# Kernel optimization log

Measured on AMD Instinct MI355X. Metric: run time of the kernel, lower is better.

The kernel has to match this reference:

```python
import jax, jax.numpy as jnp
import numpy as np

N = 8192   # max_nodes
E = 8192   # max_edges
D = 128    # node / edge feature dim


def setup_inputs() -> dict:
    key = jax.random.key(0)
    ks = jax.random.split(key, 6)
    nodes = jax.random.normal(ks[0], (N, D), jnp.float32)
    edges = jax.random.normal(ks[1], (E, D), jnp.float32)
    send = jax.random.randint(ks[2], (E,), 0, N, jnp.int32)
    rec = jax.random.randint(ks[3], (E,), 0, N, jnp.int32)
    # prefix activity masks (standard for this growing-graph module)
    anodes = (jnp.arange(N) < 6144).astype(jnp.float32)
    aedges = (jnp.arange(E) < 2048).astype(jnp.float32)
    Wq = jax.random.normal(ks[4], (D, D), jnp.float32) / np.sqrt(D)
    bq = jnp.zeros((D,), jnp.float32)
    Wp = jax.random.normal(ks[5], (D, 1), jnp.float32) * 0.1
    bp = jnp.full((1,), -5.0, jnp.float32)
    return dict(nodes=nodes, edges=edges, rec=rec, send=send, anodes=anodes,
                aedges=aedges, Wq=Wq, bq=bq, Wp=Wp, bp=bp)


def reference(nodes, edges, rec, send, anodes, aedges, Wq, bq, Wp, bp):
    # fixed PRNG key (the module takes a key argument; we pin it for determinism)
    key = jax.random.key(42)
    key_prob, key_edges, key_samp = jax.random.split(key, 3)

    nids = jnp.arange(N)
    e_active = aedges.sum().astype(jnp.int32)

    # 1. per-node edge-generation probability: prob_fn(h_i) = sigmoid(h_i @ Wp + bp)
    probs = jax.nn.sigmoid(nodes @ Wp + bp)[:, 0]            # [N]
    # 2. sample generating nodes (only active ones)
    gens = (jax.random.uniform(key_prob, (N,)) < probs * anodes).astype(jnp.float32)

    allowed = E - e_active - 1
    n_gens = jnp.clip(gens.astype(jnp.int32).sum(), 0, allowed)

    # grow active-edge mask by n_gens via repeated (mask @ incr_matrix) clip steps
    # incr_matrix(E) = I + superdiagonal, so one step extends a prefix mask by 1
    mat_e = jnp.eye(E, dtype=jnp.float32) + jnp.eye(E, k=1, dtype=jnp.float32)
    naedges = jax.lax.fori_loop(
        0, n_gens, lambda i, x: jnp.clip(x @ mat_e, 0.0, 1.0), aedges
    ).at[-1].set(0.0)
    mask_new = naedges * (1.0 - aedges)                       # [E] newly-created slots

    # 6. new edges get random embeddings in the newly-activated slots
    new_edges = edges + jax.random.normal(key_edges, edges.shape) * mask_new[:, None]

    # cumsum-derived scatter targets: k-th generating node -> edge slot e_active+k
    gi = gens.astype(jnp.int32)
    trgets = jnp.where(gens > 0, (jnp.cumsum(gens) * gens - gens).astype(jnp.int32), -1) \
             + e_active * gi                                   # [N], -1 dropped by segment_sum

    nsend = jax.ops.segment_sum(nids, trgets, num_segments=E)
    nsend = (send * (1.0 - mask_new) + nsend).astype(jnp.int32)

    # 3-5. queries, all-pairs scores, masked categorical target sampling
    queries = nodes @ Wq + bq                                  # [N, D]
    scores = jnp.clip(queries @ nodes.T, -1e4, 1e4)            # [N, N]
    scores = scores - (1.0 - anodes[None, :]) * 1e10
    select = jnp.where(gens > 0,
                       jax.random.categorical(key_samp, scores, axis=-1),
                       0).astype(jnp.int32)                    # [N]

    nrec = jax.ops.segment_sum(select, trgets, num_segments=E)
    nrec = (rec * (1.0 - mask_new) + nrec).astype(jnp.int32)

    return new_edges, nsend, nrec, naedges
```

## Files before the change

### kernel.cpp

```cpp
#include <hip/hip_runtime.h>
#include <stdint.h>
#include <math.h>

#define NN 8192
#define EE 8192
#define DD 128

__host__ __device__ inline void tf2x32(uint32_t k0, uint32_t k1, uint32_t c0, uint32_t c1,
                                       uint32_t& o0, uint32_t& o1) {
  uint32_t ks[3] = {k0, k1, 0x1BD11BDAu ^ k0 ^ k1};
  uint32_t x0 = c0 + k0, x1 = c1 + k1;
  const uint32_t rot0[4] = {13u, 15u, 26u, 6u};
  const uint32_t rot1[4] = {17u, 29u, 16u, 24u};
#pragma unroll
  for (int i = 0; i < 5; ++i) {
#pragma unroll
    for (int r = 0; r < 4; ++r) {
      uint32_t d = (i & 1) ? rot1[r] : rot0[r];
      x0 += x1;
      x1 = (x1 << d) | (x1 >> (32u - d));
      x1 ^= x0;
    }
    x0 += ks[(i + 1) % 3];
    x1 += ks[(i + 2) % 3] + (uint32_t)(i + 1);
  }
  o0 = x0; o1 = x1;
}

__device__ inline uint32_t rbits32(uint32_t k0, uint32_t k1, uint32_t idx) {
  uint32_t o0, o1;
  tf2x32(k0, k1, 0u, idx, o0, o1);
  return o0 ^ o1;
}

__device__ inline float u01(uint32_t b) {
  return __uint_as_float((b >> 9) | 0x3f800000u) - 1.0f;
}

__device__ inline float erfinv_f32(float x) {
  float w = -log1pf(-x * x);
  float p;
  if (w < 5.0f) {
    w -= 2.5f;
    p = 2.81022636e-08f;
    p = fmaf(p, w, 3.43273939e-07f);
    p = fmaf(p, w, -3.5233877e-06f);
    p = fmaf(p, w, -4.39150654e-06f);
    p = fmaf(p, w, 0.00021858087f);
    p = fmaf(p, w, -0.00125372503f);
    p = fmaf(p, w, -0.00417768164f);
    p = fmaf(p, w, 0.246640727f);
    p = fmaf(p, w, 1.50140941f);
  } else {
    w = sqrtf(w) - 3.0f;
    p = -0.000200214257f;
    p = fmaf(p, w, 0.000100950558f);
    p = fmaf(p, w, 0.00134934322f);
    p = fmaf(p, w, -0.00367342844f);
    p = fmaf(p, w, 0.00573950773f);
    p = fmaf(p, w, -0.0076224613f);
    p = fmaf(p, w, 0.00943887047f);
    p = fmaf(p, w, 1.00167406f);
    p = fmaf(p, w, 2.83297682f);
  }
  return p * x;
}

__global__ __launch_bounds__(256)
void k_gens(const float* __restrict__ nodes, const float* __restrict__ Wp,
            const float* __restrict__ bp, const float* __restrict__ anodes,
            int* __restrict__ gens, uint32_t kp0, uint32_t kp1) {
  int t = blockIdx.x * 256 + threadIdx.x;
  int i = t >> 2, qd = t & 3;
  if (i >= NN) return;
  const float4* row = (const float4*)(nodes + (size_t)i * DD);
  const float4* w = (const float4*)Wp;
  float acc = 0.f;
#pragma unroll
  for (int c = 0; c < 8; ++c) {
    int k4 = qd + 4 * c;
    float4 a = row[k4], b = w[k4];
    acc = fmaf(a.x, b.x, acc); acc = fmaf(a.y, b.y, acc);
    acc = fmaf(a.z, b.z, acc); acc = fmaf(a.w, b.w, acc);
  }
  acc += __shfl_xor(acc, 1, 4);
  acc += __shfl_xor(acc, 2, 4);
  if (qd == 0) {
    float prob = 1.0f / (1.0f + expf(-(acc + bp[0])));
    uint32_t b = rbits32(kp0, kp1, (uint32_t)i);
    gens[i] = (u01(b) < prob * anodes[i]) ? 1 : 0;
  }
}

__global__ __launch_bounds__(256)
void k_scan(const float* __restrict__ aedges, const int* __restrict__ gens,
            int* __restrict__ gen_list, float* __restrict__ mask_new,
            float* __restrict__ naedges_out, int* __restrict__ scal,
            unsigned long long* __restrict__ partial) {
  __shared__ int P[EE];
  __shared__ int aux[8];
  int tid = threadIdx.x;
  int base = tid * 32;
  int lane = tid & 63, wid = tid >> 6;

  int av[32]; int aloc = 0;
  {
    const float4* a4 = (const float4*)(aedges + base);
#pragma unroll
    for (int k4 = 0; k4 < 8; ++k4) {
      float4 x = a4[k4];
      av[4 * k4 + 0] = (x.x > 0.f); av[4 * k4 + 1] = (x.y > 0.f);
      av[4 * k4 + 2] = (x.z > 0.f); av[4 * k4 + 3] = (x.w > 0.f);
    }
#pragma unroll
    for (int k = 0; k < 32; ++k) aloc += av[k];
  }
  int incl = aloc;
#pragma unroll
  for (int d = 1; d < 64; d <<= 1) {
    int o = __shfl_up(incl, d, 64);
    if (lane >= d) incl += o;
  }
  if (lane == 63) aux[wid] = incl;

  int g[32]; int gloc = 0;
  {
    const int4* g4 = (const int4*)(gens + base);
#pragma unroll
    for (int k4 = 0; k4 < 8; ++k4) {
      int4 x = g4[k4];
      g[4 * k4 + 0] = x.x; g[4 * k4 + 1] = x.y;
      g[4 * k4 + 2] = x.z; g[4 * k4 + 3] = x.w;
    }
#pragma unroll
    for (int k = 0; k < 32; ++k) gloc += g[k];
  }
  int incg = gloc;
#pragma unroll
  for (int d = 1; d < 64; d <<= 1) {
    int o = __shfl_up(incg, d, 64);
    if (lane >= d) incg += o;
  }
  if (lane == 63) aux[4 + wid] = incg;
  __syncthreads();

  int e_active = aux[0] + aux[1] + aux[2] + aux[3];
  int total = aux[4] + aux[5] + aux[6] + aux[7];
  int wpreA = 0, wpreG = 0;
  for (int ww = 0; ww < wid; ++ww) { wpreA += aux[ww]; wpreG += aux[4 + ww]; }

  {
    int run = wpreA + incl - aloc;
#pragma unroll
    for (int k = 0; k < 32; ++k) { run += av[k]; P[base + k] = run; }
  }
  {
    int rank = wpreG + incg - gloc;
#pragma unroll
    for (int k = 0; k < 32; ++k) {
      if (g[k]) {
        if (e_active + rank < EE) gen_list[rank] = base + k;
        rank++;
      }
    }
  }
  if (tid == 0) { scal[0] = e_active; scal[1] = total; }

  for (int idx = tid; idx < total * 32; idx += 256) partial[idx] = 0ull;

  int allowed = EE - e_active - 1;
  int n_gens = total;
  if (n_gens > allowed) n_gens = allowed;
  if (n_gens < 0) n_gens = 0;

  __syncthreads();
#pragma unroll
  for (int k = 0; k < 32; ++k) {
    int j = base + k;
    int lo = j - n_gens - 1;
    int wsum = P[j] - (lo >= 0 ? P[lo] : 0);
    float dil = (wsum > 0) ? 1.f : 0.f;
    if (j == EE - 1) dil = 0.f;
    naedges_out[j] = dil;
    mask_new[j] = dil * (1.0f - (float)av[k]);
  }
}

__global__ __launch_bounds__(128)
void k_queries(const float* __restrict__ nodes, const float* __restrict__ Wq,
               const float* __restrict__ bq, const int* __restrict__ gen_list,
               const int* __restrict__ scal, float* __restrict__ queries) {
  __shared__ float ni[DD];
  int tid = threadIdx.x;
  int total = scal[1];
  for (int r = blockIdx.x; r < total; r += gridDim.x) {
    int i = gen_list[r];
    ni[tid] = nodes[(size_t)i * DD + tid];
    __syncthreads();
    float acc = bq[tid];
    for (int k = 0; k < DD; ++k) acc = fmaf(ni[k], Wq[k * DD + tid], acc);
    queries[(size_t)r * DD + tid] = acc;
    __syncthreads();
  }
}

__global__ __launch_bounds__(256)
void k_score(const float* __restrict__ nodes, const float* __restrict__ anodes,
             const float* __restrict__ queries, const int* __restrict__ gen_list,
             const int* __restrict__ scal, unsigned long long* __restrict__ partial,
             uint32_t ks0, uint32_t ks1) {
  __shared__ float4 nd[32][32];
  __shared__ float q[8][DD];
  __shared__ float an[32];
  __shared__ int gi[8];
  int tid = threadIdx.x;
  int j0 = blockIdx.x * 32;
  int total = scal[1];
  int rt0 = blockIdx.y * 8;
  if (rt0 >= total) return;

  {
    int jj = tid >> 3, sub = tid & 7;
    const float4* src = (const float4*)(nodes + (size_t)(j0 + jj) * DD);
#pragma unroll
    for (int c = 0; c < 4; ++c) {
      int k4 = sub + 8 * c;
      nd[jj][k4 ^ (jj & 7)] = src[k4];
    }
    if (tid < 32) an[tid] = anodes[j0 + tid];
  }

  int rr = tid >> 5, jj = tid & 31;
  for (int rb = rt0; rb < total; rb += 8 * gridDim.y) {
    __syncthreads();
    {
      int lr = rb + (tid >> 5);
      int k4 = tid & 31;
      if (lr < total) {
        ((float4*)q[tid >> 5])[k4] = ((const float4*)(queries + (size_t)lr * DD))[k4];
        if (k4 == 0) gi[tid >> 5] = gen_list[lr];
      }
    }
    __syncthreads();

    int r = rb + rr;
    if (r < total) {
      const float4* qv = (const float4*)q[rr];
      float acc = 0.f;
#pragma unroll
      for (int k4 = 0; k4 < 32; ++k4) {
        float4 n = nd[jj][k4 ^ (jj & 7)];
        float4 qq = qv[k4];
        acc = fmaf(n.x, qq.x, acc); acc = fmaf(n.y, qq.y, acc);
        acc = fmaf(n.z, qq.z, acc); acc = fmaf(n.w, qq.w, acc);
      }
      int j = j0 + jj;
      float sc = fminf(fmaxf(acc, -1e4f), 1e4f);
      sc -= (1.0f - an[jj]) * 1e10f;
      uint32_t bidx = (uint32_t)gi[rr] * NN + (uint32_t)j;
      uint32_t b = rbits32(ks0, ks1, bidx);
      float u = fmaxf(1.17549435e-38f, u01(b));
      float gmb = -logf(-logf(u));
      float v = sc + gmb;
      int jbest = j;
#pragma unroll
      for (int m = 16; m; m >>= 1) {
        float ov = __shfl_xor(v, m, 32);
        int oj = __shfl_xor(jbest, m, 32);
        if (ov > v || (ov == v && oj < jbest)) { v = ov; jbest = oj; }
      }
      if (jj == 0) {
        uint32_t fb = __float_as_uint(v);
        fb = (fb & 0x80000000u) ? ~fb : (fb | 0x80000000u);
        unsigned long long key =
            ((unsigned long long)fb << 32) | (uint32_t)(NN - 1 - jbest);
        atomicMax(&partial[(size_t)r * 32 + (blockIdx.x >> 3)], key);
      }
    }
  }
}

__global__ __launch_bounds__(256)
void k_post(const float* __restrict__ edges, const float* __restrict__ mask_new,
            const int* __restrict__ send, const int* __restrict__ rec,
            const int* __restrict__ gen_list,
            const unsigned long long* __restrict__ partial,
            const int* __restrict__ scal,
            float* __restrict__ out_edges, float* __restrict__ out_nsend,
            float* __restrict__ out_nrec, uint32_t ke0, uint32_t ke1) {
  int t = blockIdx.x * 256 + threadIdx.x;
  int idx = t * 4;
  int e = idx >> 7;
  float m = mask_new[e];
  float4 v = ((const float4*)edges)[t];
  if (m > 0.f) {
    float* pv = &v.x;
#pragma unroll
    for (int k = 0; k < 4; ++k) {
      uint32_t b = rbits32(ke0, ke1, (uint32_t)(idx + k));
      float u = u01(b);
      float x = fmaf(u, 2.0f, -0.99999994f);
      x = fmaxf(-0.99999994f, x);
      float nrm = 1.41421354f * erfinv_f32(x);
      pv[k] += nrm * m;
    }
  }
  ((float4*)out_edges)[t] = v;

  if (t < EE) {
    int e_active = scal[0], total = scal[1];
    float mm = mask_new[t];
    float sf = (float)send[t] * (1.0f - mm);
    float rf = (float)rec[t] * (1.0f - mm);
    int r = t - e_active;
    if (r >= 0 && r < total) {
      unsigned long long best = 0ull;
      const unsigned long long* pp = partial + (size_t)r * 32;
#pragma unroll
      for (int p = 0; p < 32; ++p) { unsigned long long x = pp[p]; if (x > best) best = x; }
      int i = gen_list[r];
      int jsel = (NN - 1) - (int)(best & 0xFFFFFFFFull);
      sf += (float)i;
      rf += (float)jsel;
    }
    out_nsend[t] = (float)(int)sf;
    out_nrec[t] = (float)(int)rf;
  }
}

extern "C" void kernel_launch(void* const* d_in, const int* in_sizes, int n_in,
                              void* d_out, int out_size, void* d_ws, size_t ws_size,
                              hipStream_t stream) {
  const float* nodes  = (const float*)d_in[0];
  const float* edges  = (const float*)d_in[1];
  const int*   rec    = (const int*)d_in[2];
  const int*   send   = (const int*)d_in[3];
  const float* anodes = (const float*)d_in[4];
  const float* aedges = (const float*)d_in[5];
  const float* Wq     = (const float*)d_in[6];
  const float* bq     = (const float*)d_in[7];
  const float* Wp     = (const float*)d_in[8];
  const float* bp     = (const float*)d_in[9];

  float* out        = (float*)d_out;
  float* out_edges  = out;
  float* out_nsend  = out + (size_t)EE * DD;
  float* out_nrec   = out_nsend + EE;
  float* out_naedge = out_nrec + EE;

  char* w = (char*)d_ws;
  int*   gens     = (int*)w;
  int*   gen_list = (int*)(w + 32768);
  int*   scal     = (int*)(w + 65536);
  float* mask_new = (float*)(w + 65792);
  unsigned long long* partial = (unsigned long long*)(w + 98560);
  float* queries  = (float*)(w + 98560 + 6144 * 32 * 8);

  uint32_t kp0, kp1, ke0, ke1, ks0, ks1;
  tf2x32(0u, 42u, 0u, 0u, kp0, kp1);
  tf2x32(0u, 42u, 0u, 1u, ke0, ke1);
  tf2x32(0u, 42u, 0u, 2u, ks0, ks1);

  k_gens<<<NN * 4 / 256, 256, 0, stream>>>(nodes, Wp, bp, anodes, gens, kp0, kp1);
  k_scan<<<1, 256, 0, stream>>>(aedges, gens, gen_list, mask_new, out_naedge, scal, partial);
  k_queries<<<128, 128, 0, stream>>>(nodes, Wq, bq, gen_list, scal, queries);
  k_score<<<dim3(NN / 32, 16), 256, 0, stream>>>(nodes, anodes, queries, gen_list, scal,
                                                 partial, ks0, ks1);
  k_post<<<(EE * DD / 4) / 256, 256, 0, stream>>>(edges, mask_new, send, rec, gen_list,
                                                  partial, scal, out_edges, out_nsend,
                                                  out_nrec, ke0, ke1);
}
```

Baseline: 44.81 us.

## Fuse score and post kernels with grid-wide completion counter

Result: slower. 68.71 us (+53.4%).

```diff
diff --git a/kernel.cpp b/kernel.cpp
--- a/kernel.cpp
+++ b/kernel.cpp
@@ -5,6 +5,7 @@
 #define NN 8192
 #define EE 8192
 #define DD 128
+#define FGRID 1280
 
 __host__ __device__ inline void tf2x32(uint32_t k0, uint32_t k1, uint32_t c0, uint32_t c1,
                                        uint32_t& o0, uint32_t& o1) {
@@ -96,7 +97,7 @@
 void k_scan(const float* __restrict__ aedges, const int* __restrict__ gens,
             int* __restrict__ gen_list, float* __restrict__ mask_new,
             float* __restrict__ naedges_out, int* __restrict__ scal,
-            unsigned long long* __restrict__ partial) {
+            unsigned long long* __restrict__ partial, int* __restrict__ done) {
   __shared__ int P[EE];
   __shared__ int aux[8];
   int tid = threadIdx.x;
@@ -164,7 +165,7 @@
       }
     }
   }
-  if (tid == 0) { scal[0] = e_active; scal[1] = total; }
+  if (tid == 0) { scal[0] = e_active; scal[1] = total; *done = 0; }
 
   for (int idx = tid; idx < total * 32; idx += 256) partial[idx] = 0ull;
 
@@ -204,111 +205,122 @@
   }
 }
 
-__global__ __launch_bounds__(256)
-void k_score(const float* __restrict__ nodes, const float* __restrict__ anodes,
+__global__ __launch_bounds__(256, 5)
+void k_fused(const float* __restrict__ nodes, const float* __restrict__ anodes,
              const float* __restrict__ queries, const int* __restrict__ gen_list,
              const int* __restrict__ scal, unsigned long long* __restrict__ partial,
-             uint32_t ks0, uint32_t ks1) {
-  __shared__ float4 nd[32][32];
+             int* __restrict__ done,
+             const float* __restrict__ edges, const float* __restrict__ mask_new,
+             const int* __restrict__ send, const int* __restrict__ rec,
+             float* __restrict__ out_edges, float* __restrict__ out_nsend,
+             float* __restrict__ out_nrec,
+             uint32_t ks0, uint32_t ks1, uint32_t ke0, uint32_t ke1) {
+  __shared__ float4 nd[32 * 32];
   __shared__ float q[8][DD];
   __shared__ float an[32];
   __shared__ int gi[8];
   int tid = threadIdx.x;
-  int j0 = blockIdx.x * 32;
+  int vx = blockIdx.x;
+  int vy0 = blockIdx.y;
   int total = scal[1];
-  int rt0 = blockIdx.y * 8;
-  if (rt0 >= total) return;
-
-  {
-    int jj = tid >> 3, sub = tid & 7;
-    const float4* src = (const float4*)(nodes + (size_t)(j0 + jj) * DD);
-#pragma unroll
-    for (int c = 0; c < 4; ++c) {
-      int k4 = sub + 8 * c;
-      nd[jj][k4 ^ (jj & 7)] = src[k4];
-    }
-    if (tid < 32) an[tid] = anodes[j0 + tid];
-  }
-
-  int rr = tid >> 5, jj = tid & 31;
-  for (int rb = rt0; rb < total; rb += 8 * gridDim.y) {
+  int ntiles = (total + 7) >> 3;
+
+  if (vy0 < ntiles) {
+    int j0 = vx * 32;
+    {
+      int jj = tid >> 3, sub = tid & 7;
+      const float4* src = (const float4*)(nodes + (size_t)(j0 + jj) * DD);
+#pragma unroll
+      for (int c = 0; c < 4; ++c) {
+        int k4 = sub + 8 * c;
+        nd[jj * 32 + ((k4 + jj) & 31)] = src[k4];
+      }
+      if (tid < 32) an[tid] = anodes[j0 + tid];
+    }
+    int rr = tid >> 5, jl = tid & 31;
+    for (int vy = vy0; vy < ntiles; vy += 5) {
+      int rb = vy * 8;
+      __syncthreads();
+      {
+        int lr = rb + (tid >> 5);
+        int k4 = tid & 31;
+        if (lr < total) {
+          ((float4*)q[tid >> 5])[k4] = ((const float4*)(queries + (size_t)lr * DD))[k4];
+          if (k4 == 0) gi[tid >> 5] = gen_list[lr];
+        }
+      }
+      __syncthreads();
+
+      int r = rb + rr;
+      if (r < total) {
+        const float4* qv = (const float4*)q[rr];
+        float acc = 0.f;
+#pragma unroll
+        for (int k4 = 0; k4 < 32; ++k4) {
+          float4 n = nd[jl * 32 + ((k4 + jl) & 31)];
+          float4 qq = qv[k4];
+          acc = fmaf(n.x, qq.x, acc); acc = fmaf(n.y, qq.y, acc);
+          acc = fmaf(n.z, qq.z, acc); acc = fmaf(n.w, qq.w, acc);
+        }
+        int j = j0 + jl;
+        float sc = fminf(fmaxf(acc, -1e4f), 1e4f);
+        sc -= (1.0f - an[jl]) * 1e10f;
+        uint32_t bidx = (uint32_t)gi[rr] * NN + (uint32_t)j;
+        uint32_t b = rbits32(ks0, ks1, bidx);
+        float u = fmaxf(1.17549435e-38f, u01(b));
+        float gmb = -logf(-logf(u));
+        float v = sc + gmb;
+        int jbest = j;
+#pragma unroll
+        for (int m = 16; m; m >>= 1) {
+          float ov = __shfl_xor(v, m, 32);
+          int oj = __shfl_xor(jbest, m, 32);
+          if (ov > v || (ov == v && oj < jbest)) { v = ov; jbest = oj; }
+        }
+        if (jl == 0) {
+          uint32_t fb = __float_as_uint(v);
+          fb = (fb & 0x80000000u) ? ~fb : (fb | 0x80000000u);
+          unsigned long long key =
+              ((unsigned long long)fb << 32) | (uint32_t)(NN - 1 - jbest);
+          atomicMax(&partial[(size_t)r * 32 + (vx >> 3)], key);
+        }
+      }
+    }
     __syncthreads();
-    {
-      int lr = rb + (tid >> 5);
-      int k4 = tid & 31;
-      if (lr < total) {
-        ((float4*)q[tid >> 5])[k4] = ((const float4*)(queries + (size_t)lr * DD))[k4];
-        if (k4 == 0) gi[tid >> 5] = gen_list[lr];
-      }
+  }
+
+  if (tid == 0)
+    __hip_atomic_fetch_add(done, 1, __ATOMIC_RELEASE, __HIP_MEMORY_SCOPE_AGENT);
+
+  int bid = vy0 * 256 + vx;
+  int t = bid * 256 + tid;
+  if (t < EE * DD / 4) {
+    int idx = t * 4;
+    int e = idx >> 7;
+    float m = mask_new[e];
+    float4 v = ((const float4*)edges)[t];
+    if (m > 0.f) {
+      float* pv = &v.x;
+#pragma unroll
+      for (int k = 0; k < 4; ++k) {
+        uint32_t b = rbits32(ke0, ke1, (uint32_t)(idx + k));
+        float u = u01(b);
+        float x = fmaf(u, 2.0f, -0.99999994f);
+        x = fmaxf(-0.99999994f, x);
+        float nrm = 1.41421354f * erfinv_f32(x);
+        pv[k] += nrm * m;
+      }
+    }
+    ((float4*)out_edges)[t] = v;
+  }
+
+  if (t < EE) {
+    if (tid == 0) {
+      while (__hip_atomic_load(done, __ATOMIC_ACQUIRE, __HIP_MEMORY_SCOPE_AGENT) < FGRID)
+        __builtin_amdgcn_s_sleep(2);
     }
     __syncthreads();
-
-    int r = rb + rr;
-    if (r < total) {
-      const float4* qv = (const float4*)q[rr];
-      float acc = 0.f;
-#pragma unroll
-      for (int k4 = 0; k4 < 32; ++k4) {
-        float4 n = nd[jj][k4 ^ (jj & 7)];
-        float4 qq = qv[k4];
-        acc = fmaf(n.x, qq.x, acc); acc = fmaf(n.y, qq.y, acc);
-        acc = fmaf(n.z, qq.z, acc); acc = fmaf(n.w, qq.w, acc);
-      }
-      int j = j0 + jj;
-      float sc = fminf(fmaxf(acc, -1e4f), 1e4f);
-      sc -= (1.0f - an[jj]) * 1e10f;
-      uint32_t bidx = (uint32_t)gi[rr] * NN + (uint32_t)j;
-      uint32_t b = rbits32(ks0, ks1, bidx);
-      float u = fmaxf(1.17549435e-38f, u01(b));
-      float gmb = -logf(-logf(u));
-      float v = sc + gmb;
-      int jbest = j;
-#pragma unroll
-      for (int m = 16; m; m >>= 1) {
-        float ov = __shfl_xor(v, m, 32);
-        int oj = __shfl_xor(jbest, m, 32);
-        if (ov > v || (ov == v && oj < jbest)) { v = ov; jbest = oj; }
-      }
-      if (jj == 0) {
-        uint32_t fb = __float_as_uint(v);
-        fb = (fb & 0x80000000u) ? ~fb : (fb | 0x80000000u);
-        unsigned long long key =
-            ((unsigned long long)fb << 32) | (uint32_t)(NN - 1 - jbest);
-        atomicMax(&partial[(size_t)r * 32 + (blockIdx.x >> 3)], key);
-      }
-    }
-  }
-}
-
-__global__ __launch_bounds__(256)
-void k_post(const float* __restrict__ edges, const float* __restrict__ mask_new,
-            const int* __restrict__ send, const int* __restrict__ rec,
-            const int* __restrict__ gen_list,
-            const unsigned long long* __restrict__ partial,
-            const int* __restrict__ scal,
-            float* __restrict__ out_edges, float* __restrict__ out_nsend,
-            float* __restrict__ out_nrec, uint32_t ke0, uint32_t ke1) {
-  int t = blockIdx.x * 256 + threadIdx.x;
-  int idx = t * 4;
-  int e = idx >> 7;
-  float m = mask_new[e];
-  float4 v = ((const float4*)edges)[t];
-  if (m > 0.f) {
-    float* pv = &v.x;
-#pragma unroll
-    for (int k = 0; k < 4; ++k) {
-      uint32_t b = rbits32(ke0, ke1, (uint32_t)(idx + k));
-      float u = u01(b);
-      float x = fmaf(u, 2.0f, -0.99999994f);
-      x = fmaxf(-0.99999994f, x);
-      float nrm = 1.41421354f * erfinv_f32(x);
-      pv[k] += nrm * m;
-    }
-  }
-  ((float4*)out_edges)[t] = v;
-
-  if (t < EE) {
-    int e_active = scal[0], total = scal[1];
+    int e_active = scal[0];
     float mm = mask_new[t];
     float sf = (float)send[t] * (1.0f - mm);
     float rf = (float)rec[t] * (1.0f - mm);
@@ -317,7 +329,11 @@
       unsigned long long best = 0ull;
       const unsigned long long* pp = partial + (size_t)r * 32;
 #pragma unroll
-      for (int p = 0; p < 32; ++p) { unsigned long long x = pp[p]; if (x > best) best = x; }
+      for (int p = 0; p < 32; ++p) {
+        unsigned long long x =
+            __hip_atomic_load(&pp[p], __ATOMIC_RELAXED, __HIP_MEMORY_SCOPE_AGENT);
+        if (x > best) best = x;
+      }
       int i = gen_list[r];
       int jsel = (NN - 1) - (int)(best & 0xFFFFFFFFull);
       sf += (float)i;
@@ -352,6 +368,7 @@
   int*   gens     = (int*)w;
   int*   gen_list = (int*)(w + 32768);
   int*   scal     = (int*)(w + 65536);
+  int*   done     = (int*)(w + 65536 + 128);
   float* mask_new = (float*)(w + 65792);
   unsigned long long* partial = (unsigned long long*)(w + 98560);
   float* queries  = (float*)(w + 98560 + 6144 * 32 * 8);
@@ -362,11 +379,11 @@
   tf2x32(0u, 42u, 0u, 2u, ks0, ks1);
 
   k_gens<<<NN * 4 / 256, 256, 0, stream>>>(nodes, Wp, bp, anodes, gens, kp0, kp1);
-  k_scan<<<1, 256, 0, stream>>>(aedges, gens, gen_list, mask_new, out_naedge, scal, partial);
+  k_scan<<<1, 256, 0, stream>>>(aedges, gens, gen_list, mask_new, out_naedge, scal,
+                                partial, done);
   k_queries<<<128, 128, 0, stream>>>(nodes, Wq, bq, gen_list, scal, queries);
-  k_score<<<dim3(NN / 32, 16), 256, 0, stream>>>(nodes, anodes, queries, gen_list, scal,
-                                                 partial, ks0, ks1);
-  k_post<<<(EE * DD / 4) / 256, 256, 0, stream>>>(edges, mask_new, send, rec, gen_list,
-                                                  partial, scal, out_edges, out_nsend,
-                                                  out_nrec, ke0, ke1);
-}
+  k_fused<<<dim3(256, 5), 256, 0, stream>>>(nodes, anodes, queries, gen_list, scal,
+                                            partial, done, edges, mask_new, send, rec,
+                                            out_edges, out_nsend, out_nrec,
+                                            ks0, ks1, ke0, ke1);
+}
```
